# Performance work log

Measured on AMD Instinct MI355X. Metric: run time of the kernel, lower is better.

Reference implementation:

```python
import jax, jax.numpy as jnp
import numpy as np

NUM_HEADS = 8
GN_GROUPS = 32
GN_EPS = 1e-5


def group_norm(x, gamma, beta):
    b, c, h, w = x.shape
    xg = x.reshape(b, GN_GROUPS, c // GN_GROUPS, h, w)
    mean = xg.mean(axis=(2, 3, 4), keepdims=True)
    var = xg.var(axis=(2, 3, 4), keepdims=True)
    xn = ((xg - mean) * jax.lax.rsqrt(var + GN_EPS)).reshape(b, c, h, w)
    return xn * gamma[None, :, None, None] + beta[None, :, None, None]


def setup_inputs() -> dict:
    key = jax.random.key(0)
    ks = jax.random.split(key, 3)
    c = 512
    x = jax.random.normal(ks[0], (8, c, 32, 32), dtype=jnp.float32)
    gn_gamma = jnp.ones((c,), jnp.float32)
    gn_beta = jnp.zeros((c,), jnp.float32)
    # 1x1 conv weights stored as [out_ch, in_ch]; scaled for numerical sanity
    w_qkv = jax.random.normal(ks[1], (3 * c, c), dtype=jnp.float32) * 0.02
    b_qkv = jnp.zeros((3 * c,), jnp.float32)
    w_out = jax.random.normal(ks[2], (c, c), dtype=jnp.float32) * 0.02
    b_out = jnp.zeros((c,), jnp.float32)
    return {"x": x, "gn_gamma": gn_gamma, "gn_beta": gn_beta,
            "w_qkv": w_qkv, "b_qkv": b_qkv, "w_out": w_out, "b_out": b_out}


def reference(x, gn_gamma, gn_beta, w_qkv, b_qkv, w_out, b_out):
    b, c, h, w = x.shape
    hd = c // NUM_HEADS
    scale = 1.0 / jnp.sqrt(jnp.float32(hd))
    residual = x
    xn = group_norm(x, gn_gamma, gn_beta)
    # 1x1 conv == channel matmul: [b, 3c, h, w]
    qkv = jnp.einsum('oc,bchw->bohw', w_qkv, xn) + b_qkv[None, :, None, None]
    q, k, v = jnp.split(qkv, 3, axis=1)
    hw = h * w
    q = q.reshape(b * NUM_HEADS, hd, hw)
    k = k.reshape(b * NUM_HEADS, hd, hw)
    v = v.reshape(b * NUM_HEADS, hd, hw)
    scores = jnp.einsum('ndi,ndj->nij', q, k) * scale  # [b*nh, hw, hw]
    probs = jax.nn.softmax(scores, axis=-1)
    out = jnp.einsum('nij,ndj->nid', probs, v)          # [b*nh, hw, hd]
    out = out.transpose(0, 2, 1).reshape(b, c, h, w)
    out = jnp.einsum('oc,bchw->bohw', w_out, out) + b_out[None, :, None, None]
    return out + residual
```

## Files before the change

### kernel.cpp

```cpp
#include <hip/hip_runtime.h>
#include <math.h>

#define NHEADS 8
#define C 512
#define HW 1024
#define HD 64

typedef __bf16 bf16x8 __attribute__((ext_vector_type(8)));
typedef __bf16 bf16x4 __attribute__((ext_vector_type(4)));
typedef float f32x4 __attribute__((ext_vector_type(4)));

__global__ __launch_bounds__(256) void wcvt_kernel(const float* __restrict__ w1,
                                                   __bf16* __restrict__ o1,
                                                   const float* __restrict__ w2,
                                                   __bf16* __restrict__ o2) {
  int id = blockIdx.x * 2048 + threadIdx.x * 8;
  const float* src;
  __bf16* dst;
  int off;
  if (id < 786432) { src = w1; dst = o1; off = id; }
  else { src = w2; dst = o2; off = id - 786432; }
  float4 a = *(const float4*)(src + off);
  float4 b = *(const float4*)(src + off + 4);
  bf16x8 o;
  o[0] = (__bf16)a.x; o[1] = (__bf16)a.y; o[2] = (__bf16)a.z; o[3] = (__bf16)a.w;
  o[4] = (__bf16)b.x; o[5] = (__bf16)b.y; o[6] = (__bf16)b.z; o[7] = (__bf16)b.w;
  *(bf16x8*)(dst + off) = o;
}

__global__ __launch_bounds__(256) void gn_kernel(const float* __restrict__ x,
                                                 const float* __restrict__ gamma,
                                                 const float* __restrict__ beta,
                                                 __bf16* __restrict__ xnT) {
  int b = blockIdx.x >> 5, g = blockIdx.x & 31;
  const size_t base = ((size_t)b * C + (size_t)g * 16) * HW;
  const float4* xp = (const float4*)(x + base);
  int tid = threadIdx.x;

  float s = 0.f, ss = 0.f;
  float4 v[16];
#pragma unroll
  for (int it = 0; it < 16; it++) {
    v[it] = xp[tid + it * 256];
    s += v[it].x + v[it].y + v[it].z + v[it].w;
    ss += v[it].x * v[it].x + v[it].y * v[it].y + v[it].z * v[it].z + v[it].w * v[it].w;
  }
#pragma unroll
  for (int off = 32; off > 0; off >>= 1) {
    s += __shfl_down(s, off);
    ss += __shfl_down(ss, off);
  }
  __shared__ float red[8];
  __shared__ float mi[2];
  int wid = tid >> 6;
  if ((tid & 63) == 0) { red[wid] = s; red[4 + wid] = ss; }
  __syncthreads();
  if (tid == 0) {
    float S = red[0] + red[1] + red[2] + red[3];
    float SS = red[4] + red[5] + red[6] + red[7];
    float mean = S * (1.f / 16384.f);
    float var = SS * (1.f / 16384.f) - mean * mean;
    mi[0] = mean;
    mi[1] = rsqrtf(var + 1e-5f);
  }
  __syncthreads();
  float mean = mi[0], inv = mi[1];
  float ga[16], be[16];
#pragma unroll
  for (int it = 0; it < 16; it++) {
    float g_ = gamma[g * 16 + it] * inv;
    ga[it] = g_;
    be[it] = beta[g * 16 + it] - mean * g_;
  }
  __bf16* dstb = xnT + ((size_t)b * HW + (size_t)tid * 4) * C + g * 16;
#pragma unroll
  for (int jj = 0; jj < 4; jj++) {
    bf16x8 w0, w1;
#pragma unroll
    for (int e = 0; e < 8; e++) {
      w0[e] = (__bf16)(((const float*)&v[e])[jj] * ga[e] + be[e]);
      w1[e] = (__bf16)(((const float*)&v[e + 8])[jj] * ga[e + 8] + be[e + 8]);
    }
    *(bf16x8*)(dstb + (size_t)jj * C) = w0;
    *(bf16x8*)(dstb + (size_t)jj * C + 8) = w1;
  }
}

template <int EPI>
__global__ __launch_bounds__(256) void gemm_rr(const __bf16* __restrict__ Rp, size_t Rbs,
                                               const __bf16* __restrict__ Cp, size_t Cbs,
                                               const float* __restrict__ bias,
                                               __bf16* __restrict__ q_or_v,
                                               __bf16* __restrict__ kT,
                                               const float* __restrict__ resid,
                                               float* __restrict__ Yout) {
  int bx = blockIdx.x, by = blockIdx.y, b = blockIdx.z;
  int tid = threadIdx.x, wid = tid >> 6, lane = tid & 63;
  int l15 = lane & 15, lhi = lane >> 4;
  int wr = wid >> 1, wc = wid & 1;

  const __bf16* Rb = Rp + (size_t)b * Rbs + (size_t)by * 128 * 512;
  const __bf16* Cb = Cp + (size_t)b * Cbs + (size_t)bx * 128 * 512;

  __shared__ __align__(16) char smem[32768];
  char* Rs = smem;
  char* Cs = smem + 16384;

  f32x4 acc[4][4] = {};
  int srow = tid >> 1, sc0 = (tid & 1) * 4;

  for (int kk = 0; kk < 512; kk += 64) {
    __syncthreads();
    const __bf16* rg = Rb + (size_t)srow * 512 + kk + sc0 * 8;
    const __bf16* cg = Cb + (size_t)srow * 512 + kk + sc0 * 8;
#pragma unroll
    for (int q = 0; q < 4; q++) {
      int c = sc0 + q;
      int o = srow * 128 + ((c ^ (srow & 7)) << 4);
      *(uint4*)(Rs + o) = *(const uint4*)(rg + q * 8);
      *(uint4*)(Cs + o) = *(const uint4*)(cg + q * 8);
    }
    __syncthreads();
#pragma unroll
    for (int ks = 0; ks < 2; ks++) {
      bf16x8 ar[4], br[4];
      int c = ks * 4 + lhi;
#pragma unroll
      for (int m = 0; m < 4; m++) {
        int row = wr * 64 + m * 16 + l15;
        ar[m] = *(const bf16x8*)(Rs + row * 128 + ((c ^ (row & 7)) << 4));
      }
#pragma unroll
      for (int n = 0; n < 4; n++) {
        int row = wc * 64 + n * 16 + l15;
        br[n] = *(const bf16x8*)(Cs + row * 128 + ((c ^ (row & 7)) << 4));
      }
#pragma unroll
      for (int m = 0; m < 4; m++)
#pragma unroll
        for (int n = 0; n < 4; n++)
          acc[m][n] = __builtin_amdgcn_mfma_f32_16x16x32_bf16(ar[m], br[n], acc[m][n], 0, 0, 0);
    }
  }

  int rbase = by * 128 + wr * 64;
  int cbase = bx * 128 + wc * 64;

  if (EPI == 0) {
#pragma unroll
    for (int n = 0; n < 4; n++) {
      int col = cbase + n * 16 + l15;
      int sec = col >> 9;
      int h = (col >> 6) & 7;
      int d = col & 63;
      __bf16* dst0 = (sec ? kT : q_or_v) + ((size_t)b * 8 + h) * (size_t)(HW * HD) + d;
      float bs = bias[col];
#pragma unroll
      for (int m = 0; m < 4; m++)
#pragma unroll
        for (int r = 0; r < 4; r++) {
          int i = rbase + m * 16 + lhi * 4 + r;
          dst0[(size_t)i * HD] = (__bf16)(acc[m][n][r] + bs);
        }
    }
  } else if (EPI == 1) {
#pragma unroll
    for (int m = 0; m < 4; m++)
#pragma unroll
      for (int r = 0; r < 4; r++) {
        int row = rbase + m * 16 + lhi * 4 + r;
        int h = row >> 6, d = row & 63;
        float bs = bias[row];
        __bf16* dst = q_or_v + (((size_t)b * 8 + h) * HD + d) * HW;
#pragma unroll
        for (int n = 0; n < 4; n++) {
          int j = cbase + n * 16 + l15;
          dst[j] = (__bf16)(acc[m][n][r] + bs);
        }
      }
  } else {
#pragma unroll
    for (int m = 0; m < 4; m++)
#pragma unroll
      for (int r = 0; r < 4; r++) {
        int o = rbase + m * 16 + lhi * 4 + r;
        float bs = bias[o];
        size_t base2 = ((size_t)b * C + o) * HW;
#pragma unroll
        for (int n = 0; n < 4; n++) {
          int j = cbase + n * 16 + l15;
          Yout[base2 + j] = acc[m][n][r] + bs + resid[base2 + j];
        }
      }
  }
}

__global__ __launch_bounds__(256) void attn_mfma_kernel(const __bf16* __restrict__ qT,
                                                        const __bf16* __restrict__ kT,
                                                        const __bf16* __restrict__ vN,
                                                        __bf16* __restrict__ aT) {
  int bh = blockIdx.x & 63;
  int qt = blockIdx.x >> 6;
  int tid = threadIdx.x;
  int wid = tid >> 6;
  int lane = tid & 63;
  int l15 = lane & 15;
  int lhi = lane >> 4;

  const __bf16* qh = qT + (size_t)bh * HW * HD;
  const char* kh = (const char*)(kT + (size_t)bh * HW * HD);
  const char* vh = (const char*)(vN + (size_t)bh * HD * HW);

  __shared__ __align__(16) char smem[49152];
  char* pb = smem + 32768 + wid * 4096;

  int i0 = qt * 128 + wid * 32;

  bf16x8 qf[2][2];
#pragma unroll
  for (int it = 0; it < 2; it++)
#pragma unroll
    for (int ks = 0; ks < 2; ks++) {
      int row = i0 + it * 16 + l15;
      bf16x8 qv = *(const bf16x8*)(qh + (size_t)row * HD + ks * 32 + lhi * 8);
#pragma unroll
      for (int e = 0; e < 8; e++) qv[e] = (__bf16)((float)qv[e] * 0.125f);
      qf[it][ks] = qv;
    }

  int sr = tid >> 3, sc = tid & 7;
  int sr2 = sr + 32;
  int swz1 = sr * 128 + ((sc ^ (sr & 7)) << 4);
  int swz2 = sr2 * 128 + ((sc ^ (sr2 & 7)) << 4);

  uint4 kr0, kr1, vr0, vr1;
  {
    kr0 = *(const uint4*)(kh + (size_t)sr * 128 + sc * 16);
    kr1 = *(const uint4*)(kh + (size_t)sr2 * 128 + sc * 16);
    vr0 = *(const uint4*)(vh + (size_t)sr * 2048 + sc * 16);
    vr1 = *(const uint4*)(vh + (size_t)sr2 * 2048 + sc * 16);
    *(uint4*)(smem + swz1) = kr0;
    *(uint4*)(smem + swz2) = kr1;
    *(uint4*)(smem + 8192 + swz1) = vr0;
    *(uint4*)(smem + 8192 + swz2) = vr1;
  }

  f32x4 accO[2][4] = {};
  f32x4 lacc[2] = {};
  float m[2][4];
#pragma unroll
  for (int it = 0; it < 2; it++)
#pragma unroll
    for (int r = 0; r < 4; r++) m[it][r] = -1e30f;

  bf16x8 ones;
#pragma unroll
  for (int e = 0; e < 8; e++) ones[e] = (__bf16)1.0f;

  for (int t = 0; t < 16; ++t) {
    if (t < 15) {
      int j0n = (t + 1) * 64;
      kr0 = *(const uint4*)(kh + (size_t)(j0n + sr) * 128 + sc * 16);
      kr1 = *(const uint4*)(kh + (size_t)(j0n + sr2) * 128 + sc * 16);
      vr0 = *(const uint4*)(vh + (size_t)sr * 2048 + j0n * 2 + sc * 16);
      vr1 = *(const uint4*)(vh + (size_t)sr2 * 2048 + j0n * 2 + sc * 16);
    }
    __syncthreads();
    const char* kt = smem + ((t & 1) << 14);
    const char* vt = kt + 8192;

    f32x4 s_[2][4] = {};
#pragma unroll
    for (int ks = 0; ks < 2; ++ks)
#pragma unroll
      for (int jt = 0; jt < 4; ++jt) {
        int j = jt * 16 + l15;
        int c = ks * 4 + lhi;
        bf16x8 bk = *(const bf16x8*)(kt + j * 128 + ((c ^ (j & 7)) << 4));
        s_[0][jt] = __builtin_amdgcn_mfma_f32_16x16x32_bf16(qf[0][ks], bk, s_[0][jt], 0, 0, 0);
        s_[1][jt] = __builtin_amdgcn_mfma_f32_16x16x32_bf16(qf[1][ks], bk, s_[1][jt], 0, 0, 0);
      }

    float lm[2][4];
    int ok = 1;
#pragma unroll
    for (int it = 0; it < 2; ++it)
#pragma unroll
      for (int r = 0; r < 4; r++) {
        lm[it][r] = fmaxf(fmaxf(s_[it][0][r], s_[it][1][r]),
                          fmaxf(s_[it][2][r], s_[it][3][r]));
        ok &= (lm[it][r] <= m[it][r] + 8.f);
      }
    if (!__all(ok)) {
#pragma unroll
      for (int it = 0; it < 2; ++it) {
        float pm[4];
#pragma unroll
        for (int r = 0; r < 4; r++) pm[r] = lm[it][r];
#pragma unroll
        for (int off = 1; off < 16; off <<= 1)
#pragma unroll
          for (int r = 0; r < 4; r++) pm[r] = fmaxf(pm[r], __shfl_xor(pm[r], off));
#pragma unroll
        for (int r = 0; r < 4; r++) {
          float nm = fmaxf(m[it][r], pm[r]);
          float corr = __expf(m[it][r] - nm);
          m[it][r] = nm;
          lacc[it][r] *= corr;
#pragma unroll
          for (int dt = 0; dt < 4; ++dt) accO[it][dt][r] *= corr;
        }
      }
    }
#pragma unroll
    for (int it = 0; it < 2; ++it)
#pragma unroll
      for (int jt = 0; jt < 4; ++jt)
#pragma unroll
        for (int r = 0; r < 4; r++) {
          float p = __expf(s_[it][jt][r] - m[it][r]);
          int row = it * 16 + lhi * 4 + r;
          int j = jt * 16 + l15;
          int off2 = row * 128 + (((j >> 3) ^ (row & 7)) << 4) + (j & 7) * 2;
          *(__bf16*)(pb + off2) = (__bf16)p;
        }

#pragma unroll
    for (int kj = 0; kj < 2; ++kj) {
      bf16x8 pa[2];
#pragma unroll
      for (int it = 0; it < 2; ++it) {
        int row = it * 16 + l15;
        int c = kj * 4 + lhi;
        pa[it] = *(const bf16x8*)(pb + row * 128 + ((c ^ (row & 7)) << 4));
      }
      lacc[0] = __builtin_amdgcn_mfma_f32_16x16x32_bf16(pa[0], ones, lacc[0], 0, 0, 0);
      lacc[1] = __builtin_amdgcn_mfma_f32_16x16x32_bf16(pa[1], ones, lacc[1], 0, 0, 0);
#pragma unroll
      for (int dt = 0; dt < 4; ++dt) {
        int d = dt * 16 + l15;
        int c = kj * 4 + lhi;
        bf16x8 bv = *(const bf16x8*)(vt + d * 128 + ((c ^ (d & 7)) << 4));
        accO[0][dt] = __builtin_amdgcn_mfma_f32_16x16x32_bf16(pa[0], bv, accO[0][dt], 0, 0, 0);
        accO[1][dt] = __builtin_amdgcn_mfma_f32_16x16x32_bf16(pa[1], bv, accO[1][dt], 0, 0, 0);
      }
    }

    if (t < 15) {
      char* ktn = smem + (((t + 1) & 1) << 14);
      *(uint4*)(ktn + swz1) = kr0;
      *(uint4*)(ktn + swz2) = kr1;
      *(uint4*)(ktn + 8192 + swz1) = vr0;
      *(uint4*)(ktn + 8192 + swz2) = vr1;
    }
  }

  __syncthreads();
  __bf16* Lo = (__bf16*)(smem + wid * 4608);
#pragma unroll
  for (int it = 0; it < 2; ++it)
#pragma unroll
    for (int r = 0; r < 4; r++) {
      float inv = 1.f / lacc[it][r];
      int iloc = it * 16 + lhi * 4 + r;
#pragma unroll
      for (int dt = 0; dt < 4; ++dt)
        Lo[iloc * 72 + dt * 16 + l15] = (__bf16)(accO[it][dt][r] * inv);
    }
  __syncthreads();
  int b = bh >> 3, hh = bh & 7;
  int iloc = lane >> 1, dh = (lane & 1) * 32;
  __bf16* dst = aT + ((size_t)b * HW + i0 + iloc) * C + hh * 64 + dh;
  const __bf16* srcl = Lo + iloc * 72 + dh;
#pragma unroll
  for (int s2 = 0; s2 < 4; s2++)
    *(uint4*)(dst + s2 * 8) = *(const uint4*)(srcl + s2 * 8);
}

extern "C" void kernel_launch(void* const* d_in, const int* in_sizes, int n_in,
                              void* d_out, int out_size, void* d_ws, size_t ws_size,
                              hipStream_t stream) {
  const float* x = (const float*)d_in[0];
  const float* gamma = (const float*)d_in[1];
  const float* beta = (const float*)d_in[2];
  const float* w_qkv = (const float*)d_in[3];
  const float* b_qkv = (const float*)d_in[4];
  const float* w_out = (const float*)d_in[5];
  const float* b_out = (const float*)d_in[6];
  float* out = (float*)d_out;

  char* ws = (char*)d_ws;
  const size_t MB = 1024 * 1024;
  __bf16* xnT = (__bf16*)ws;
  __bf16* qT  = (__bf16*)(ws + 8 * MB);
  __bf16* kT  = (__bf16*)(ws + 16 * MB);
  __bf16* vN  = (__bf16*)(ws + 24 * MB);
  __bf16* aT  = (__bf16*)(ws + 32 * MB);
  __bf16* wbq = (__bf16*)(ws + 40 * MB);
  __bf16* wbo = (__bf16*)(ws + 42 * MB);

  wcvt_kernel<<<dim3(512), 256, 0, stream>>>(w_qkv, wbq, w_out, wbo);
  gn_kernel<<<dim3(256), 256, 0, stream>>>(x, gamma, beta, xnT);
  gemm_rr<0><<<dim3(8, 8, 8), 256, 0, stream>>>(xnT, (size_t)HW * C, wbq, 0,
                                                b_qkv, qT, kT, nullptr, nullptr);
  gemm_rr<1><<<dim3(8, 4, 8), 256, 0, stream>>>(wbq + (size_t)1024 * 512, 0, xnT, (size_t)HW * C,
                                                b_qkv + 1024, vN, nullptr, nullptr, nullptr);
  attn_mfma_kernel<<<dim3(512), 256, 0, stream>>>(qT, kT, vN, aT);
  gemm_rr<2><<<dim3(8, 4, 8), 256, 0, stream>>>(wbo, 0, aT, (size_t)HW * C,
                                                b_out, nullptr, nullptr, x, out);
}
```

Before: 173.2 us.

## Double-buffer GEMM shared tiles with register prefetch; use exp2 softmax with folded log2e

The 1x1-conv GEMM now holds two shared-memory tile buffers and prefetches the next K-slice from global memory into registers while the current slice's MFMAs run. It then writes those registers to the other buffer, which drops one barrier per iteration. Separately, the attention kernel folds log2(e) into the Q scale and replaces __expf with exp2f to save a multiply per exponent. The GEMM's shared memory doubles to 64KB, which may lower occupancy, and the online-softmax threshold of 8 now applies in log2 units.

```diff
diff --git a/kernel.cpp b/kernel.cpp
--- a/kernel.cpp
+++ b/kernel.cpp
@@ -102,25 +102,40 @@
   const __bf16* Rb = Rp + (size_t)b * Rbs + (size_t)by * 128 * 512;
   const __bf16* Cb = Cp + (size_t)b * Cbs + (size_t)bx * 128 * 512;
 
-  __shared__ __align__(16) char smem[32768];
-  char* Rs = smem;
-  char* Cs = smem + 16384;
+  __shared__ __align__(16) char smem[65536];
 
   f32x4 acc[4][4] = {};
   int srow = tid >> 1, sc0 = (tid & 1) * 4;
 
-  for (int kk = 0; kk < 512; kk += 64) {
+  int soff[4];
+#pragma unroll
+  for (int q = 0; q < 4; q++)
+    soff[q] = srow * 128 + (((sc0 + q) ^ (srow & 7)) << 4);
+
+  uint4 rr[4], cr[4];
+#pragma unroll
+  for (int q = 0; q < 4; q++) {
+    rr[q] = *(const uint4*)(Rb + (size_t)srow * 512 + (sc0 + q) * 8);
+    cr[q] = *(const uint4*)(Cb + (size_t)srow * 512 + (sc0 + q) * 8);
+  }
+#pragma unroll
+  for (int q = 0; q < 4; q++) {
+    *(uint4*)(smem + soff[q]) = rr[q];
+    *(uint4*)(smem + 16384 + soff[q]) = cr[q];
+  }
+
+  for (int kk8 = 0; kk8 < 8; kk8++) {
+    if (kk8 < 7) {
+      int kk = (kk8 + 1) * 64;
+#pragma unroll
+      for (int q = 0; q < 4; q++) {
+        rr[q] = *(const uint4*)(Rb + (size_t)srow * 512 + kk + (sc0 + q) * 8);
+        cr[q] = *(const uint4*)(Cb + (size_t)srow * 512 + kk + (sc0 + q) * 8);
+      }
+    }
     __syncthreads();
-    const __bf16* rg = Rb + (size_t)srow * 512 + kk + sc0 * 8;
-    const __bf16* cg = Cb + (size_t)srow * 512 + kk + sc0 * 8;
-#pragma unroll
-    for (int q = 0; q < 4; q++) {
-      int c = sc0 + q;
-      int o = srow * 128 + ((c ^ (srow & 7)) << 4);
-      *(uint4*)(Rs + o) = *(const uint4*)(rg + q * 8);
-      *(uint4*)(Cs + o) = *(const uint4*)(cg + q * 8);
-    }
-    __syncthreads();
+    const char* Rs = smem + ((kk8 & 1) << 15);
+    const char* Cs = Rs + 16384;
 #pragma unroll
     for (int ks = 0; ks < 2; ks++) {
       bf16x8 ar[4], br[4];
@@ -140,6 +155,14 @@
 #pragma unroll
         for (int n = 0; n < 4; n++)
           acc[m][n] = __builtin_amdgcn_mfma_f32_16x16x32_bf16(ar[m], br[n], acc[m][n], 0, 0, 0);
+    }
+    if (kk8 < 7) {
+      char* Rd = smem + (((kk8 + 1) & 1) << 15);
+#pragma unroll
+      for (int q = 0; q < 4; q++) {
+        *(uint4*)(Rd + soff[q]) = rr[q];
+        *(uint4*)(Rd + 16384 + soff[q]) = cr[q];
+      }
     }
   }
 
@@ -224,7 +247,7 @@
       int row = i0 + it * 16 + l15;
       bf16x8 qv = *(const bf16x8*)(qh + (size_t)row * HD + ks * 32 + lhi * 8);
 #pragma unroll
-      for (int e = 0; e < 8; e++) qv[e] = (__bf16)((float)qv[e] * 0.125f);
+      for (int e = 0; e < 8; e++) qv[e] = (__bf16)((float)qv[e] * 0.180336884f);
       qf[it][ks] = qv;
     }
 
@@ -304,7 +327,7 @@
 #pragma unroll
         for (int r = 0; r < 4; r++) {
           float nm = fmaxf(m[it][r], pm[r]);
-          float corr = __expf(m[it][r] - nm);
+          float corr = exp2f(m[it][r] - nm);
           m[it][r] = nm;
           lacc[it][r] *= corr;
 #pragma unroll
@@ -318,7 +341,7 @@
       for (int jt = 0; jt < 4; ++jt)
 #pragma unroll
         for (int r = 0; r < 4; r++) {
-          float p = __expf(s_[it][jt][r] - m[it][r]);
+          float p = exp2f(s_[it][jt][r] - m[it][r]);
           int row = it * 16 + lhi * 4 + r;
           int j = jt * 16 + l15;
           int off2 = row * 128 + (((j >> 3) ^ (row & 7)) << 4) + (j & 7) * 2;
```

Measured after the change: 293.8 us. 1.7x slower.
